# Kernel tuning notes

Hardware: AMD Instinct MI355X
Metric: run time of the kernel (lower is better)

The kernel has to match this reference:

```python
import jax, jax.numpy as jnp
import numpy as np

N_USERS = 100000
N_ITEMS = 200000
NNZ = 5000000
DIM = 64
N_LAYERS = 3
ALPHA = 0.5


def setup_inputs() -> dict:
    key = jax.random.key(0)
    ks = jax.random.split(key, 9)
    N = N_USERS + N_ITEMS
    users = jax.random.randint(ks[0], (4096,), 0, N_USERS, dtype=jnp.int64 if jax.config.jax_enable_x64 else jnp.int32)
    items = jax.random.randint(ks[1], (4096,), 0, N_ITEMS, dtype=users.dtype)
    rows = jax.random.randint(ks[2], (NNZ,), 0, N, dtype=users.dtype)
    cols = jax.random.randint(ks[3], (NNZ,), 0, N, dtype=users.dtype)
    vals = jax.random.uniform(ks[4], (NNZ,), dtype=jnp.float32)
    user_emb = jax.random.normal(ks[5], (N_USERS, DIM), dtype=jnp.float32)
    item_emb = jax.random.normal(ks[6], (N_ITEMS, DIM), dtype=jnp.float32)
    user_emb0 = jax.random.normal(ks[7], (N_USERS, DIM), dtype=jnp.float32)
    item_emb0 = jax.random.normal(ks[8], (N_ITEMS, DIM), dtype=jnp.float32)
    return {"users": users, "items": items, "rows": rows, "cols": cols,
            "vals": vals, "user_emb": user_emb, "item_emb": item_emb,
            "user_emb0": user_emb0, "item_emb0": item_emb0}


def _computer(vals, user_emb, item_emb, user_emb0, item_emb0, rows, cols):
    # LightGCN propagation with scaled SVD residual (VS_LightGCN.computer)
    N = user_emb.shape[0] + item_emb.shape[0]
    all_emb = jnp.concatenate([user_emb, item_emb], axis=0)      # [N, D]
    all_emb0 = jnp.concatenate([user_emb0, item_emb0], axis=0)   # [N, D]
    embs = [all_emb]
    for layer in range(N_LAYERS):
        # SpMM: out[r] = sum_{e: rows[e]==r} vals[e] * all_emb[cols[e]]
        msg = vals[:, None] * all_emb[cols]                      # [nnz, D]
        all_emb = jax.ops.segment_sum(msg, rows, num_segments=N) + ALPHA * all_emb0
        embs.append((N_LAYERS - layer) * all_emb)
    light_out = jnp.mean(jnp.stack(embs, axis=1), axis=1)        # [N, D]
    return light_out


def reference(users, items, rows, cols, vals, user_emb, item_emb, user_emb0, item_emb0):
    light_out = _computer(vals, user_emb, item_emb, user_emb0, item_emb0, rows, cols)
    users_emb = light_out[users]                                 # [B, D]
    items_emb = light_out[user_emb.shape[0] + items]             # [B, D]
    gamma = jnp.sum(users_emb * items_emb, axis=1)               # [B]
    return gamma
```

## Files before the change

### kernel.cpp

```cpp
#include <hip/hip_runtime.h>

#define ALPHA 0.5f
#define BSHIFT 11
#define RPB 2048
#define MAXB 256
#define PCHUNK 16384


__device__ __forceinline__ float bf2f(unsigned short u) {
  return __uint_as_float((unsigned)u << 16);
}
__device__ __forceinline__ unsigned short f2bf(float f) {
  unsigned u = __float_as_uint(f);
  u += 0x7fffu + ((u >> 16) & 1u);
  return (unsigned short)(u >> 16);
}


__global__ __launch_bounds__(256) void k_count(
    const int* __restrict__ rows, int nnz, int* __restrict__ bcnt) {
  __shared__ int lcnt[MAXB];
  int t = threadIdx.x;
  if (t < MAXB) lcnt[t] = 0;
  __syncthreads();
  int stride = 512 * 256;
  for (int e = blockIdx.x * 256 + t; e < nnz; e += stride)
    atomicAdd(&lcnt[rows[e] >> BSHIFT], 1);
  __syncthreads();
  if (t < MAXB) {
    int c = lcnt[t];
    if (c) atomicAdd(&bcnt[t], c);
  }
}


__global__ void k_scan_buckets(const int* __restrict__ bcnt, int nb,
                               int* __restrict__ bptr, int* __restrict__ bcur) {
  __shared__ int s[256];
  int t = threadIdx.x;
  int v = (t < nb) ? bcnt[t] : 0;
  s[t] = v; __syncthreads();
  for (int d = 1; d < 256; d <<= 1) {
    int x = (t >= d) ? s[t - d] : 0;
    __syncthreads();
    s[t] += x;
    __syncthreads();
  }
  if (t < nb) {
    int excl = s[t] - v;
    bptr[t] = excl;
    bcur[t] = excl;
  }
  if (t == 0) bptr[nb] = s[255];
}


__global__ __launch_bounds__(1024) void k_part_conv(
    const int* __restrict__ rows, const int* __restrict__ cols, const float* __restrict__ vals,
    int nnz, int* __restrict__ bcur, uint2* __restrict__ pPay, int PB,
    const float* __restrict__ uE, const float* __restrict__ iE,
    int nU64, int nTot, unsigned short* __restrict__ out) {
  __shared__ int lcnt[MAXB];
  __shared__ int lbase[MAXB];
  int t = threadIdx.x;
  if ((int)blockIdx.x < PB) {
    if (t < MAXB) lcnt[t] = 0;
    __syncthreads();
    int base = blockIdx.x * PCHUNK;
    int end = nnz < base + PCHUNK ? nnz : base + PCHUNK;
    for (int e = base + t; e < end; e += 1024)
      atomicAdd(&lcnt[rows[e] >> BSHIFT], 1);
    __syncthreads();
    if (t < MAXB) {
      int c = lcnt[t];
      lbase[t] = c ? atomicAdd(&bcur[t], c) : 0;
      lcnt[t] = 0;
    }
    __syncthreads();
    for (int e = base + t; e < end; e += 1024) {
      int r = rows[e];
      int b = r >> BSHIFT;
      int p = lbase[b] + atomicAdd(&lcnt[b], 1);
      uint2 pay;
      pay.x = ((unsigned)(r & (RPB - 1)) << 20) | (unsigned)cols[e];
      pay.y = __float_as_uint(vals[e]);
      pPay[p] = pay;
    }
  } else {
    int i = (((int)blockIdx.x - PB) * 1024 + t) * 4;
    if (i >= nTot) return;
    const float* src = (i < nU64) ? (uE + i) : (iE + (i - nU64));
    float4 v = *(const float4*)src;
    ushort4 o;
    o.x = f2bf(v.x); o.y = f2bf(v.y); o.z = f2bf(v.z); o.w = f2bf(v.w);
    *(ushort4*)(out + i) = o;
  }
}


__global__ __launch_bounds__(1024) void k_build_csr(
    const int* __restrict__ bptr, const uint2* __restrict__ pPay, int N,
    int* __restrict__ rowptr, int* __restrict__ cnt, int2* __restrict__ colval,
    int* __restrict__ degHist) {
  __shared__ int lcnt[RPB];
  __shared__ int scanbuf[1024];
  __shared__ int ldeg[256];
  int t = threadIdx.x;
  int b = blockIdx.x;
  int r0 = b << BSHIFT;
  int rCount = N - r0; if (rCount > RPB) rCount = RPB;
  int eBeg = bptr[b], eEnd = bptr[b + 1];

  for (int r = t; r < RPB; r += 1024) lcnt[r] = 0;
  if (t < 256) ldeg[t] = 0;
  __syncthreads();
  for (int e = eBeg + t; e < eEnd; e += 1024)
    atomicAdd(&lcnt[pPay[e].x >> 20], 1);
  __syncthreads();
  for (int r = t; r < rCount; r += 1024) {
    int c = lcnt[r];
    cnt[r0 + r] = c;
    atomicAdd(&ldeg[c < 255 ? c : 255], 1);
  }
  int v2[2]; int s = 0;
#pragma unroll
  for (int k = 0; k < 2; k++) {
    int x = lcnt[2 * t + k];
    v2[k] = s; s += x;
  }
  scanbuf[t] = s; __syncthreads();
  for (int d = 1; d < 1024; d <<= 1) {
    int x = (t >= d) ? scanbuf[t - d] : 0;
    __syncthreads();
    scanbuf[t] += x;
    __syncthreads();
  }
  int blockExcl = scanbuf[t] - s;
#pragma unroll
  for (int k = 0; k < 2; k++) lcnt[2 * t + k] = blockExcl + v2[k];
  __syncthreads();
  if (t < 256 && ldeg[t]) atomicAdd(&degHist[t], ldeg[t]);
  for (int r = t; r < rCount; r += 1024) rowptr[r0 + r] = eBeg + lcnt[r];
  __syncthreads();
  for (int e = eBeg + t; e < eEnd; e += 1024) {
    uint2 pay = pPay[e];
    int r = (int)(pay.x >> 20);
    int p = eBeg + atomicAdd(&lcnt[r], 1);
    int2 cv; cv.x = (int)(pay.x & 0xFFFFFu); cv.y = (int)pay.y;
    colval[p] = cv;
  }
}


__global__ void k_degscan(const int* __restrict__ degHist, int* __restrict__ degCur,
                          int2* __restrict__ colval, int nnz) {
  __shared__ int s[256];
  int t = threadIdx.x;
  int v = degHist[t];
  s[t] = v; __syncthreads();
  for (int d = 1; d < 256; d <<= 1) {
    int x = (t >= d) ? s[t - d] : 0;
    __syncthreads();
    s[t] += x;
    __syncthreads();
  }
  degCur[t] = s[t] - v;
  if (t < 8) { int2 z; z.x = 0; z.y = 0; colval[nnz + t] = z; }
}


__global__ __launch_bounds__(256) void k_permute(
    const int* __restrict__ rowptr, const int* __restrict__ cnt, int N,
    int* __restrict__ degCur,
    int* __restrict__ perm, int* __restrict__ rowptrS, int* __restrict__ lenS) {
  __shared__ int lcnt[256];
  __shared__ int lbase[256];
  int t = threadIdx.x;
  lcnt[t] = 0;
  __syncthreads();
  int base = blockIdx.x * 1024;
  int end = N < base + 1024 ? N : base + 1024;
  for (int r = base + t; r < end; r += 256) {
    int c = cnt[r];
    atomicAdd(&lcnt[c < 255 ? c : 255], 1);
  }
  __syncthreads();
  {
    int c = lcnt[t];
    lbase[t] = c ? atomicAdd(&degCur[t], c) : 0;
    lcnt[t] = 0;
  }
  __syncthreads();
  for (int r = base + t; r < end; r += 256) {
    int c = cnt[r];
    int bin = c < 255 ? c : 255;
    int pos = lbase[bin] + atomicAdd(&lcnt[bin], 1);
    perm[pos] = r;
    rowptrS[pos] = rowptr[r];
    lenS[pos] = c;
  }
}


__device__ __forceinline__ void spmm_body(
    int gtid,
    const unsigned short* __restrict__ src,
    const float* __restrict__ e0U, const float* __restrict__ e0I, int split,
    const int* __restrict__ perm, const int* __restrict__ rowptrS, const int* __restrict__ lenS,
    const int2* __restrict__ colval,
    unsigned short* __restrict__ dst, int n) {
  int wave = gtid >> 6;
  int lane = gtid & 63;
  int sub = lane >> 4;
  int k   = lane & 15;
  int q = wave * 4 + sub;
  int s0 = 2 * q, s1 = 2 * q + 1;
  bool va = s0 < n, vb = s1 < n;
  int i0 = va ? s0 : 0, i1 = vb ? s1 : 0;
  int row0 = perm[i0], row1 = perm[i1];
  int st0 = rowptrS[i0], st1 = rowptrS[i1];
  int len0 = va ? lenS[i0] : 0, len1 = vb ? lenS[i1] : 0;
  const int2* cv0 = colval + st0;
  const int2* cv1 = colval + st1;
  const unsigned short* srcK = src + (size_t)k * 4;
  int l0m = len0 > 0 ? len0 - 1 : 0;
  int l1m = len1 > 0 ? len1 - 1 : 0;
  int mx = max(len0, len1);

  float p0 = 0.f, p1 = 0.f, p2 = 0.f, p3 = 0.f;
  float r0a = 0.f, r1a = 0.f, r2a = 0.f, r3a = 0.f;
  for (int j = 0; j < mx; j += 2) {
    int ja = j, jb = j + 1;
    int j0a = ja < l0m ? ja : l0m, j0b = jb < l0m ? jb : l0m;
    int j1a = ja < l1m ? ja : l1m, j1b = jb < l1m ? jb : l1m;
    int2 e0a = cv0[j0a];
    int2 e0b = cv0[j0b];
    int2 e1a = cv1[j1a];
    int2 e1b = cv1[j1b];
    ushort4 x0a = *(const ushort4*)(srcK + (size_t)e0a.x * 64);
    ushort4 x0b = *(const ushort4*)(srcK + (size_t)e0b.x * 64);
    ushort4 x1a = *(const ushort4*)(srcK + (size_t)e1a.x * 64);
    ushort4 x1b = *(const ushort4*)(srcK + (size_t)e1b.x * 64);
    float w0a = ja < len0 ? __int_as_float(e0a.y) : 0.f;
    float w0b = jb < len0 ? __int_as_float(e0b.y) : 0.f;
    float w1a = ja < len1 ? __int_as_float(e1a.y) : 0.f;
    float w1b = jb < len1 ? __int_as_float(e1b.y) : 0.f;
    p0 = fmaf(w0a, bf2f(x0a.x), p0); p1 = fmaf(w0a, bf2f(x0a.y), p1);
    p2 = fmaf(w0a, bf2f(x0a.z), p2); p3 = fmaf(w0a, bf2f(x0a.w), p3);
    p0 = fmaf(w0b, bf2f(x0b.x), p0); p1 = fmaf(w0b, bf2f(x0b.y), p1);
    p2 = fmaf(w0b, bf2f(x0b.z), p2); p3 = fmaf(w0b, bf2f(x0b.w), p3);
    r0a = fmaf(w1a, bf2f(x1a.x), r0a); r1a = fmaf(w1a, bf2f(x1a.y), r1a);
    r2a = fmaf(w1a, bf2f(x1a.z), r2a); r3a = fmaf(w1a, bf2f(x1a.w), r3a);
    r0a = fmaf(w1b, bf2f(x1b.x), r0a); r1a = fmaf(w1b, bf2f(x1b.y), r1a);
    r2a = fmaf(w1b, bf2f(x1b.z), r2a); r3a = fmaf(w1b, bf2f(x1b.w), r3a);
  }
  if (va) {
    const float* e0p = (row0 < split) ? (e0U + (size_t)row0 * 64)
                                      : (e0I + (size_t)(row0 - split) * 64);
    float4 ev = *(const float4*)(e0p + k * 4);
    ushort4 o;
    o.x = f2bf(p0 + ALPHA * ev.x);
    o.y = f2bf(p1 + ALPHA * ev.y);
    o.z = f2bf(p2 + ALPHA * ev.z);
    o.w = f2bf(p3 + ALPHA * ev.w);
    *(ushort4*)(dst + (size_t)row0 * 64 + k * 4) = o;
  }
  if (vb) {
    const float* e0p = (row1 < split) ? (e0U + (size_t)row1 * 64)
                                      : (e0I + (size_t)(row1 - split) * 64);
    float4 ev = *(const float4*)(e0p + k * 4);
    ushort4 o;
    o.x = f2bf(r0a + ALPHA * ev.x);
    o.y = f2bf(r1a + ALPHA * ev.y);
    o.z = f2bf(r2a + ALPHA * ev.z);
    o.w = f2bf(r3a + ALPHA * ev.w);
    *(ushort4*)(dst + (size_t)row1 * 64 + k * 4) = o;
  }
}


__global__ __launch_bounds__(256) void k_spmm1_mark(
    const unsigned short* __restrict__ src,
    const float* __restrict__ e0U, const float* __restrict__ e0I, int split,
    const int* __restrict__ perm, const int* __restrict__ rowptrS, const int* __restrict__ lenS,
    const int2* __restrict__ colval,
    unsigned short* __restrict__ dst, int n, int MB,
    const int* __restrict__ users, const int* __restrict__ items, int B,
    const int* __restrict__ rowptr, const int* __restrict__ cnt,
    unsigned char* __restrict__ flag) {
  if ((int)blockIdx.x < MB) {
    int t = (int)blockIdx.x * 256 + threadIdx.x;
    int wave = t >> 6;
    int lane = t & 63;
    int sub = lane >> 4;
    int k = lane & 15;
    int idx = wave * 4 + sub;
    if (idx >= 2 * B) return;
    int row = (idx < B) ? users[idx] : split + items[idx - B];
    if (k == 0) flag[row] = 1;
    int start = rowptr[row], len = cnt[row];
    for (int j = k; j < len; j += 16) flag[colval[start + j].x] = 1;
  } else {
    spmm_body((int)((blockIdx.x - MB) * 256 + threadIdx.x), src, e0U, e0I, split,
              perm, rowptrS, lenS, colval, dst, n);
  }
}


__global__ __launch_bounds__(1024) void k_compact(
    const int* __restrict__ perm, const int* __restrict__ rowptrS, const int* __restrict__ lenS,
    const unsigned char* __restrict__ flag, int N, int* __restrict__ selTotal,
    int* __restrict__ selPerm, int* __restrict__ selRowptrS, int* __restrict__ selLenS) {
  __shared__ int sbuf[1024];
  __shared__ int sbase;
  int t = threadIdx.x;
  int i = (int)blockIdx.x * 1024 + t;
  int f = 0, r = 0, rp = 0, ln = 0;
  if (i < N) {
    r = perm[i];
    f = flag[r];
    if (f) { rp = rowptrS[i]; ln = lenS[i]; }
  }
  sbuf[t] = f; __syncthreads();
  for (int d = 1; d < 1024; d <<= 1) {
    int x = (t >= d) ? sbuf[t - d] : 0;
    __syncthreads();
    sbuf[t] += x;
    __syncthreads();
  }
  int incl = sbuf[t];
  if (t == 1023) sbase = atomicAdd(selTotal, incl);
  __syncthreads();
  if (f) {
    int pos = sbase + incl - 1;
    selPerm[pos] = r;
    selRowptrS[pos] = rp;
    selLenS[pos] = ln;
  }
}

__global__ __launch_bounds__(256) void k_spmm2_acc(
    const unsigned short* __restrict__ ebA,
    const float* __restrict__ e0U, const float* __restrict__ e0I, int split,
    const int* __restrict__ selPerm, const int* __restrict__ selRowptrS,
    const int* __restrict__ selLenS, const int* __restrict__ nSelPtr,
    const int2* __restrict__ colval,
    unsigned short* __restrict__ ebB, int spmmBlocks,
    const int* __restrict__ users, const int* __restrict__ items, int B,
    const float* __restrict__ user_emb, const float* __restrict__ item_emb,
    float* __restrict__ accU, float* __restrict__ accI) {
  if ((int)blockIdx.x < spmmBlocks) {
    int nSel = *nSelPtr;
    spmm_body((int)(blockIdx.x * 256 + threadIdx.x), ebA, e0U, e0I, split,
              selPerm, selRowptrS, selLenS, colval, ebB, nSel);
  } else {
    int t = ((int)blockIdx.x - spmmBlocks) * 256 + threadIdx.x;
    int total = B * 64;
    if (t < total) {
      int b = t >> 6, d = t & 63;
      size_t idx = (size_t)users[b] * 64 + d;
      accU[t] = user_emb[idx] + 3.f * bf2f(ebA[idx]);
    } else if (t < 2 * total) {
      int t2 = t - total;
      int b = t2 >> 6, d = t2 & 63;
      int r = items[b];
      accI[t2] = item_emb[(size_t)r * 64 + d] + 3.f * bf2f(ebA[(size_t)(split + r) * 64 + d]);
    }
  }
}


__global__ __launch_bounds__(256) void k_mini3(
    const int* __restrict__ users, const int* __restrict__ items, int B, int split,
    const unsigned short* __restrict__ ebB,
    const float* __restrict__ e0U, const float* __restrict__ e0I,
    const int* __restrict__ rowptr, const int* __restrict__ cnt,
    const int2* __restrict__ colval,
    float* __restrict__ accU, float* __restrict__ accI) {
  int wave = (int)((blockIdx.x * blockDim.x + threadIdx.x) >> 6);
  int lane = threadIdx.x & 63;
  int sub = lane >> 4;
  int k   = lane & 15;
  int idx = wave * 4 + sub;
  bool valid = idx < 2 * B;
  int ic = valid ? idx : 0;
  int row;
  float* accp;
  if (ic < B) { row = users[ic];             accp = accU + (size_t)ic * 64; }
  else        { row = split + items[ic - B]; accp = accI + (size_t)(ic - B) * 64; }
  int start = rowptr[row];
  int len   = valid ? cnt[row] : 0;
  int maxlen = len;
  maxlen = max(maxlen, __shfl_xor(maxlen, 16));
  maxlen = max(maxlen, __shfl_xor(maxlen, 32));
  const int2* cv = colval + start;
  const unsigned short* srcK = ebB + (size_t)k * 4;

  float a0 = 0.f, a1 = 0.f, a2 = 0.f, a3 = 0.f;
  for (int j = 0; j < maxlen; j += 4) {
#pragma unroll
    for (int u = 0; u < 4; u++) {
      int jj = j + u;
      if (jj < len) {
        int2 e = cv[jj];
        float v = __int_as_float(e.y);
        ushort4 x = *(const ushort4*)(srcK + (size_t)e.x * 64);
        a0 = fmaf(v, bf2f(x.x), a0);
        a1 = fmaf(v, bf2f(x.y), a1);
        a2 = fmaf(v, bf2f(x.z), a2);
        a3 = fmaf(v, bf2f(x.w), a3);
      }
    }
  }
  if (valid) {
    const float* e0p = (row < split) ? (e0U + (size_t)row * 64)
                                     : (e0I + (size_t)(row - split) * 64);
    float4 ev = *(const float4*)(e0p + k * 4);
    ushort4 x2 = *(const ushort4*)(srcK + (size_t)row * 64);
    float4 cur = *(const float4*)(accp + k * 4);
    cur.x += a0 + ALPHA * ev.x + 2.f * bf2f(x2.x);
    cur.y += a1 + ALPHA * ev.y + 2.f * bf2f(x2.y);
    cur.z += a2 + ALPHA * ev.z + 2.f * bf2f(x2.z);
    cur.w += a3 + ALPHA * ev.w + 2.f * bf2f(x2.w);
    *(float4*)(accp + k * 4) = cur;
  }
}

__global__ void k_dot(const float* __restrict__ accU, const float* __restrict__ accI, int B,
                      float* __restrict__ out) {
  int wave = (int)((blockIdx.x * blockDim.x + threadIdx.x) >> 6);
  int lane = threadIdx.x & 63;
  if (wave >= B) return;
  float p = accU[(size_t)wave * 64 + lane] * accI[(size_t)wave * 64 + lane];
  for (int d = 32; d > 0; d >>= 1) p += __shfl_xor(p, d);
  if (lane == 0) out[wave] = p * (1.f / 16.f);
}


extern "C" void kernel_launch(void* const* d_in, const int* in_sizes, int n_in,
                              void* d_out, int out_size, void* d_ws, size_t ws_size,
                              hipStream_t stream) {
  const int*   users     = (const int*)d_in[0];
  const int*   items     = (const int*)d_in[1];
  const int*   rows      = (const int*)d_in[2];
  const int*   cols      = (const int*)d_in[3];
  const float* vals      = (const float*)d_in[4];
  const float* user_emb  = (const float*)d_in[5];
  const float* item_emb  = (const float*)d_in[6];
  const float* user_emb0 = (const float*)d_in[7];
  const float* item_emb0 = (const float*)d_in[8];
  float* gamma = (float*)d_out;

  int B   = in_sizes[0];
  int nnz = in_sizes[2];
  int nU  = in_sizes[5] / 64;
  int nI  = in_sizes[6] / 64;
  int N   = nU + nI;
  int nb  = (N + RPB - 1) >> BSHIFT;
  int Nf  = (N + 15) & ~15;

  char* base = (char*)d_ws;
  unsigned short* ebIn = (unsigned short*)base;
  unsigned short* ebA  = ebIn + (size_t)N * 64;
  unsigned short* ebB  = ebA  + (size_t)N * 64;
  uint2* pPay = (uint2*)ebA;
  char* p = (char*)(ebB + (size_t)N * 64);
  int2* colval  = (int2*)p;           p += ((size_t)nnz + 8) * sizeof(int2);
  int*  rowptr  = (int*)p;            p += (size_t)N * sizeof(int);
  int*  cnt     = (int*)p;            p += (size_t)N * sizeof(int);
  int*  perm    = (int*)p;            p += (size_t)N * sizeof(int);
  int*  rowptrS = (int*)p;            p += (size_t)N * sizeof(int);
  int*  lenS    = (int*)p;            p += (size_t)N * sizeof(int);
  int*  selPerm    = (int*)p;         p += (size_t)N * sizeof(int);
  int*  selRowptrS = (int*)p;         p += (size_t)N * sizeof(int);
  int*  selLenS    = (int*)p;         p += (size_t)N * sizeof(int);
  int*  bcnt    = (int*)p;            p += MAXB * sizeof(int);
  int*  degHist = (int*)p;            p += 256 * sizeof(int);
  int*  selTotal= (int*)p;            p += 4 * sizeof(int);
  unsigned char* flag = (unsigned char*)p; p += Nf;
  int*  bptr    = (int*)p;            p += (MAXB + 1) * sizeof(int);
  int*  bcur    = (int*)p;            p += MAXB * sizeof(int);
  int*  degCur  = (int*)p;            p += 256 * sizeof(int);
  float* accU   = (float*)p;          p += (size_t)B * 64 * sizeof(float);
  float* accI   = (float*)p;          p += (size_t)B * 64 * sizeof(float);

  hipMemsetAsync(bcnt, 0, (MAXB + 256 + 4) * sizeof(int) + Nf, stream);

  const int tpb = 256;
  int nTot = N * 64;

  k_count<<<512, tpb, 0, stream>>>(rows, nnz, bcnt);
  k_scan_buckets<<<1, 256, 0, stream>>>(bcnt, nb, bptr, bcur);

  int PB = (nnz + PCHUNK - 1) / PCHUNK;
  int convB = (nTot / 4 + 1023) / 1024;
  k_part_conv<<<PB + convB, 1024, 0, stream>>>(rows, cols, vals, nnz, bcur, pPay, PB,
                                               user_emb, item_emb, nU * 64, nTot, ebIn);

  k_build_csr<<<nb, 1024, 0, stream>>>(bptr, pPay, N, rowptr, cnt, colval, degHist);
  k_degscan<<<1, 256, 0, stream>>>(degHist, degCur, colval, nnz);
  k_permute<<<(N + 1023) / 1024, tpb, 0, stream>>>(rowptr, cnt, N, degCur, perm, rowptrS, lenS);

  int spmmBlocks = (N + 31) / 32;
  int accBlocks = (2 * B * 64 + tpb - 1) / tpb;
  int markBlocks = (2 * B + 15) / 16;

  k_spmm1_mark<<<markBlocks + spmmBlocks, tpb, 0, stream>>>(
      ebIn, user_emb0, item_emb0, nU, perm, rowptrS, lenS, colval, ebA, N,
      markBlocks, users, items, B, rowptr, cnt, flag);

  k_compact<<<(N + 1023) / 1024, 1024, 0, stream>>>(perm, rowptrS, lenS, flag, N,
                                                    selTotal, selPerm, selRowptrS, selLenS);

  k_spmm2_acc<<<spmmBlocks + accBlocks, tpb, 0, stream>>>(
      ebA, user_emb0, item_emb0, nU, selPerm, selRowptrS, selLenS, selTotal,
      colval, ebB, spmmBlocks, users, items, B, user_emb, item_emb, accU, accI);

  int mBlocks = (2 * B + 15) / 16;
  k_mini3<<<mBlocks, tpb, 0, stream>>>(users, items, B, nU, ebB,
                                       user_emb0, item_emb0,
                                       rowptr, cnt, colval, accU, accI);

  k_dot<<<(B * 64 + tpb - 1) / tpb, tpb, 0, stream>>>(accU, accI, B, gamma);
}
```

Measured before the change: 564.6 us.

## Replace bucket count and atomic partition with per-chunk histogram scan and finer buckets

The COO-to-CSR build now computes a per-chunk bucket histogram, does a column-wise prefix scan in one block, and scatters with precomputed per-chunk offsets. This replaces the global-atomic bucket cursors and the duplicate count pass inside the partition kernel. Buckets shrink from 2048 to 512 rows, giving about 586 build_csr blocks instead of 147 for more parallelism, and chunks double to 32768. In exchange the single-block scan walks roughly 153 chunks serially per bucket, and build_csr blocks of 1024 threads now scan only 512 rows.

```diff
diff --git a/kernel.cpp b/kernel.cpp
--- a/kernel.cpp
+++ b/kernel.cpp
@@ -1,10 +1,10 @@
 #include <hip/hip_runtime.h>
 
 #define ALPHA 0.5f
-#define BSHIFT 11
-#define RPB 2048
-#define MAXB 256
-#define PCHUNK 16384
+#define BSHIFT 9
+#define RPB 512
+#define NBMAX 640
+#define PCHUNK 32768
 
 
 __device__ __forceinline__ float bf2f(unsigned short u) {
@@ -17,66 +17,64 @@
 }
 
 
-__global__ __launch_bounds__(256) void k_count(
-    const int* __restrict__ rows, int nnz, int* __restrict__ bcnt) {
-  __shared__ int lcnt[MAXB];
-  int t = threadIdx.x;
-  if (t < MAXB) lcnt[t] = 0;
-  __syncthreads();
-  int stride = 512 * 256;
-  for (int e = blockIdx.x * 256 + t; e < nnz; e += stride)
+__global__ __launch_bounds__(1024) void k_hist(
+    const int* __restrict__ rows, int nnz, int* __restrict__ histG, int nb) {
+  __shared__ int lcnt[NBMAX];
+  int t = threadIdx.x;
+  if (t < nb) lcnt[t] = 0;
+  __syncthreads();
+  int base = blockIdx.x * PCHUNK;
+  int end = nnz < base + PCHUNK ? nnz : base + PCHUNK;
+  for (int e = base + t; e < end; e += 1024)
     atomicAdd(&lcnt[rows[e] >> BSHIFT], 1);
   __syncthreads();
-  if (t < MAXB) {
-    int c = lcnt[t];
-    if (c) atomicAdd(&bcnt[t], c);
-  }
-}
-
-
-__global__ void k_scan_buckets(const int* __restrict__ bcnt, int nb,
-                               int* __restrict__ bptr, int* __restrict__ bcur) {
-  __shared__ int s[256];
-  int t = threadIdx.x;
-  int v = (t < nb) ? bcnt[t] : 0;
-  s[t] = v; __syncthreads();
-  for (int d = 1; d < 256; d <<= 1) {
-    int x = (t >= d) ? s[t - d] : 0;
-    __syncthreads();
-    s[t] += x;
-    __syncthreads();
-  }
+  if (t < nb) histG[(size_t)blockIdx.x * nb + t] = lcnt[t];
+}
+
+
+__global__ __launch_bounds__(1024) void k_scanh(
+    int* __restrict__ histG, int nb, int nchunks, int nnz, int* __restrict__ bptr) {
+  __shared__ int tot[1024];
+  int t = threadIdx.x;
+  int total = 0;
   if (t < nb) {
-    int excl = s[t] - v;
-    bptr[t] = excl;
-    bcur[t] = excl;
-  }
-  if (t == 0) bptr[nb] = s[255];
-}
-
-
-__global__ __launch_bounds__(1024) void k_part_conv(
+    for (int c = 0; c < nchunks; c++) {
+      int idx = c * nb + t;
+      int v = histG[idx];
+      histG[idx] = total;
+      total += v;
+    }
+  }
+  tot[t] = (t < nb) ? total : 0;
+  __syncthreads();
+  for (int d = 1; d < 1024; d <<= 1) {
+    int x = (t >= d) ? tot[t - d] : 0;
+    __syncthreads();
+    tot[t] += x;
+    __syncthreads();
+  }
+  if (t < nb) bptr[t] = tot[t] - total;
+  if (t == 0) bptr[nb] = nnz;
+}
+
+
+__global__ __launch_bounds__(1024) void k_scatter_conv(
     const int* __restrict__ rows, const int* __restrict__ cols, const float* __restrict__ vals,
-    int nnz, int* __restrict__ bcur, uint2* __restrict__ pPay, int PB,
+    int nnz, int nb, const int* __restrict__ bptr, const int* __restrict__ histG,
+    uint2* __restrict__ pPay, int PB,
     const float* __restrict__ uE, const float* __restrict__ iE,
     int nU64, int nTot, unsigned short* __restrict__ out) {
-  __shared__ int lcnt[MAXB];
-  __shared__ int lbase[MAXB];
+  __shared__ int lbase[NBMAX];
+  __shared__ int lcnt[NBMAX];
   int t = threadIdx.x;
   if ((int)blockIdx.x < PB) {
-    if (t < MAXB) lcnt[t] = 0;
+    if (t < nb) {
+      lbase[t] = bptr[t] + histG[(size_t)blockIdx.x * nb + t];
+      lcnt[t] = 0;
+    }
     __syncthreads();
     int base = blockIdx.x * PCHUNK;
     int end = nnz < base + PCHUNK ? nnz : base + PCHUNK;
-    for (int e = base + t; e < end; e += 1024)
-      atomicAdd(&lcnt[rows[e] >> BSHIFT], 1);
-    __syncthreads();
-    if (t < MAXB) {
-      int c = lcnt[t];
-      lbase[t] = c ? atomicAdd(&bcur[t], c) : 0;
-      lcnt[t] = 0;
-    }
-    __syncthreads();
     for (int e = base + t; e < end; e += 1024) {
       int r = rows[e];
       int b = r >> BSHIFT;
@@ -103,7 +101,7 @@
     int* __restrict__ rowptr, int* __restrict__ cnt, int2* __restrict__ colval,
     int* __restrict__ degHist) {
   __shared__ int lcnt[RPB];
-  __shared__ int scanbuf[1024];
+  __shared__ int scanbuf[RPB];
   __shared__ int ldeg[256];
   int t = threadIdx.x;
   int b = blockIdx.x;
@@ -111,36 +109,31 @@
   int rCount = N - r0; if (rCount > RPB) rCount = RPB;
   int eBeg = bptr[b], eEnd = bptr[b + 1];
 
-  for (int r = t; r < RPB; r += 1024) lcnt[r] = 0;
+  if (t < RPB) lcnt[t] = 0;
   if (t < 256) ldeg[t] = 0;
   __syncthreads();
   for (int e = eBeg + t; e < eEnd; e += 1024)
     atomicAdd(&lcnt[pPay[e].x >> 20], 1);
   __syncthreads();
-  for (int r = t; r < rCount; r += 1024) {
-    int c = lcnt[r];
-    cnt[r0 + r] = c;
-    atomicAdd(&ldeg[c < 255 ? c : 255], 1);
-  }
-  int v2[2]; int s = 0;
-#pragma unroll
-  for (int k = 0; k < 2; k++) {
-    int x = lcnt[2 * t + k];
-    v2[k] = s; s += x;
-  }
-  scanbuf[t] = s; __syncthreads();
-  for (int d = 1; d < 1024; d <<= 1) {
-    int x = (t >= d) ? scanbuf[t - d] : 0;
-    __syncthreads();
-    scanbuf[t] += x;
-    __syncthreads();
-  }
-  int blockExcl = scanbuf[t] - s;
-#pragma unroll
-  for (int k = 0; k < 2; k++) lcnt[2 * t + k] = blockExcl + v2[k];
+  int c0 = 0;
+  if (t < rCount) {
+    c0 = lcnt[t];
+    cnt[r0 + t] = c0;
+    atomicAdd(&ldeg[c0 < 255 ? c0 : 255], 1);
+  }
+  int s = 0;
+  if (t < RPB) { s = lcnt[t]; scanbuf[t] = s; }
+  __syncthreads();
+  for (int d = 1; d < RPB; d <<= 1) {
+    int x = (t >= d && t < RPB) ? scanbuf[t - d] : 0;
+    __syncthreads();
+    if (t < RPB) scanbuf[t] += x;
+    __syncthreads();
+  }
+  if (t < RPB) lcnt[t] = scanbuf[t] - s;
   __syncthreads();
   if (t < 256 && ldeg[t]) atomicAdd(&degHist[t], ldeg[t]);
-  for (int r = t; r < rCount; r += 1024) rowptr[r0 + r] = eBeg + lcnt[r];
+  if (t < rCount) rowptr[r0 + t] = eBeg + lcnt[t];
   __syncthreads();
   for (int e = eBeg + t; e < eEnd; e += 1024) {
     uint2 pay = pPay[e];
@@ -457,6 +450,7 @@
   int nI  = in_sizes[6] / 64;
   int N   = nU + nI;
   int nb  = (N + RPB - 1) >> BSHIFT;
+  int PB  = (nnz + PCHUNK - 1) / PCHUNK;
   int Nf  = (N + 15) & ~15;
 
   char* base = (char*)d_ws;
@@ -474,28 +468,27 @@
   int*  selPerm    = (int*)p;         p += (size_t)N * sizeof(int);
   int*  selRowptrS = (int*)p;         p += (size_t)N * sizeof(int);
   int*  selLenS    = (int*)p;         p += (size_t)N * sizeof(int);
-  int*  bcnt    = (int*)p;            p += MAXB * sizeof(int);
+  int*  histG   = (int*)p;            p += (size_t)PB * nb * sizeof(int);
+  int*  bptr    = (int*)p;            p += (nb + 1) * sizeof(int);
   int*  degHist = (int*)p;            p += 256 * sizeof(int);
   int*  selTotal= (int*)p;            p += 4 * sizeof(int);
   unsigned char* flag = (unsigned char*)p; p += Nf;
-  int*  bptr    = (int*)p;            p += (MAXB + 1) * sizeof(int);
-  int*  bcur    = (int*)p;            p += MAXB * sizeof(int);
   int*  degCur  = (int*)p;            p += 256 * sizeof(int);
   float* accU   = (float*)p;          p += (size_t)B * 64 * sizeof(float);
   float* accI   = (float*)p;          p += (size_t)B * 64 * sizeof(float);
 
-  hipMemsetAsync(bcnt, 0, (MAXB + 256 + 4) * sizeof(int) + Nf, stream);
+  hipMemsetAsync(degHist, 0, (256 + 4) * sizeof(int) + Nf, stream);
 
   const int tpb = 256;
   int nTot = N * 64;
 
-  k_count<<<512, tpb, 0, stream>>>(rows, nnz, bcnt);
-  k_scan_buckets<<<1, 256, 0, stream>>>(bcnt, nb, bptr, bcur);
-
-  int PB = (nnz + PCHUNK - 1) / PCHUNK;
+  k_hist<<<PB, 1024, 0, stream>>>(rows, nnz, histG, nb);
+  k_scanh<<<1, 1024, 0, stream>>>(histG, nb, PB, nnz, bptr);
+
   int convB = (nTot / 4 + 1023) / 1024;
-  k_part_conv<<<PB + convB, 1024, 0, stream>>>(rows, cols, vals, nnz, bcur, pPay, PB,
-                                               user_emb, item_emb, nU * 64, nTot, ebIn);
+  k_scatter_conv<<<PB + convB, 1024, 0, stream>>>(rows, cols, vals, nnz, nb, bptr, histG,
+                                                  pPay, PB, user_emb, item_emb,
+                                                  nU * 64, nTot, ebIn);
 
   k_build_csr<<<nb, 1024, 0, stream>>>(bptr, pPay, N, rowptr, cnt, colval, degHist);
   k_degscan<<<1, 256, 0, stream>>>(degHist, degCur, colval, nnz);
```

Result: slower. 591.3 us (+4.7%).
